# Performance work log

Hardware: AMD Instinct MI355X
Metric: run time of the kernel (lower is better)

Reference implementation:

```python
import jax, jax.numpy as jnp
import numpy as np

B, H, W, C = 16, 256, 256, 3
K_MAX = 64


def setup_inputs() -> dict:
    key = jax.random.key(0)
    k1, k2, k3 = jax.random.split(key, 3)
    images = jax.random.uniform(k1, (B, H, W, C), dtype=jnp.float32)
    palettes = jax.random.uniform(k2, (B, K_MAX, C), dtype=jnp.float32)
    # ragged palette sizes in [1, K_MAX]; entries >= size are padding
    palette_sizes = jax.random.randint(k3, (B,), 1, K_MAX + 1, dtype=jnp.int32)
    temperature = jnp.float32(1.0)
    return {"images": images, "palettes": palettes,
            "palette_sizes": palette_sizes, "temperature": temperature}


def reference(images, palettes, palette_sizes, temperature):
    # valid-entry mask emulating the ragged [B, (K), C] palette
    mask = jnp.arange(K_MAX)[None, :] < palette_sizes[:, None]          # [B, K]
    # per-pixel squared distance to each palette color: [B, H, W, K]
    diff = images[:, :, :, None, :] - palettes[:, None, None, :, :]
    distances = jnp.sum(diff * diff, axis=-1)
    logits = -distances / temperature
    # padded palette slots get -inf logits -> zero softmax weight,
    # exactly matching the ragged softmax over K_i entries
    logits = jnp.where(mask[:, None, None, :], logits, -jnp.inf)
    weights = jax.nn.softmax(logits, axis=-1)                            # [B, H, W, K]
    # softmax-weighted color blend (padded slots contribute 0)
    return jnp.einsum('bhwk,bkc->bhwc', weights, palettes)
```

## Files before the change

### kernel.cpp

```cpp
#include <hip/hip_runtime.h>


#define BATCH 16
#define HW 65536
#define KMAX 64
#define BLOCKS_PER_IMG 256

__global__ __launch_bounds__(64) void coef_kernel(
    const float* __restrict__ palettes,
    const float* __restrict__ temperature,
    float*       __restrict__ cf)
{
    const int b = blockIdx.x;
    const int k = threadIdx.x;
    const float invT  = 1.0f / temperature[0];
    const float scale = invT * 1.4426950408889634f;

    const float pr = palettes[(b * KMAX + k) * 3 + 0];
    const float pg = palettes[(b * KMAX + k) * 3 + 1];
    const float pb = palettes[(b * KMAX + k) * 3 + 2];

    float* o = cf + ((long)(b * KMAX + k) << 3);
    o[0] = 2.0f * pr * scale;
    o[1] = 2.0f * pg * scale;
    o[2] = 2.0f * pb * scale;
    o[3] = (-(pr * pr + pg * pg + pb * pb) - 3.0f) * scale;
    o[4] = pr;
    o[5] = pg;
    o[6] = pb;
    o[7] = 0.0f;
}

__global__ __launch_bounds__(256) void palette_blend_kernel(
    const float* __restrict__ images,
    const int*   __restrict__ palette_sizes,
    const float* __restrict__ cf,
    float*       __restrict__ out)
{
    const int b   = blockIdx.x >> 8;
    const int pix = ((blockIdx.x & (BLOCKS_PER_IMG - 1)) << 8) + threadIdx.x;
    const int K   = palette_sizes[b];

    const long base = (long)b * (HW * 3) + (long)pix * 3;
    const float x0 = images[base + 0];
    const float x1 = images[base + 1];
    const float x2 = images[base + 2];

    const float4* __restrict__ c4 = (const float4*)(cf + ((long)b * KMAX << 3));

    float s = 0.0f, o0 = 0.0f, o1 = 0.0f, o2 = 0.0f;
    #pragma unroll 4
    for (int k = 0; k < K; ++k) {
        const float4 A = c4[2 * k];
        const float4 P = c4[2 * k + 1];
        const float l2 = fmaf(A.x, x0, fmaf(A.y, x1, fmaf(A.z, x2, A.w)));
        const float w  = exp2f(l2);
        s  += w;
        o0 = fmaf(w, P.x, o0);
        o1 = fmaf(w, P.y, o1);
        o2 = fmaf(w, P.z, o2);
    }

    const float inv = 1.0f / s;
    out[base + 0] = o0 * inv;
    out[base + 1] = o1 * inv;
    out[base + 2] = o2 * inv;
}

extern "C" void kernel_launch(void* const* d_in, const int* in_sizes, int n_in,
                              void* d_out, int out_size, void* d_ws, size_t ws_size,
                              hipStream_t stream) {
    const float* images        = (const float*)d_in[0];
    const float* palettes      = (const float*)d_in[1];
    const int*   palette_sizes = (const int*)d_in[2];
    const float* temperature   = (const float*)d_in[3];
    float*       out           = (float*)d_out;
    float*       cf            = (float*)d_ws;

    coef_kernel<<<dim3(BATCH), dim3(KMAX), 0, stream>>>(palettes, temperature, cf);
    palette_blend_kernel<<<dim3(BATCH * BLOCKS_PER_IMG), dim3(256), 0, stream>>>(
        images, palette_sizes, cf, out);
}
```

Measured before the change: 84.14 us.

## Move palette coefficients to constant memory and drop duplicate palette colors

```diff
diff --git a/kernel.cpp b/kernel.cpp
--- a/kernel.cpp
+++ b/kernel.cpp
@@ -5,6 +5,9 @@
 #define HW 65536
 #define KMAX 64
 #define BLOCKS_PER_IMG 256
+#define CF_ELEMS (BATCH * KMAX * 4)
+
+__constant__ float cf_const[CF_ELEMS];
 
 __global__ __launch_bounds__(64) void coef_kernel(
     const float* __restrict__ palettes,
@@ -13,28 +16,23 @@
 {
     const int b = blockIdx.x;
     const int k = threadIdx.x;
-    const float invT  = 1.0f / temperature[0];
-    const float scale = invT * 1.4426950408889634f;
+    const float scale = 1.4426950408889634f / temperature[0];
 
     const float pr = palettes[(b * KMAX + k) * 3 + 0];
     const float pg = palettes[(b * KMAX + k) * 3 + 1];
     const float pb = palettes[(b * KMAX + k) * 3 + 2];
 
-    float* o = cf + ((long)(b * KMAX + k) << 3);
+    float* o = cf + ((b * KMAX + k) << 2);
     o[0] = 2.0f * pr * scale;
     o[1] = 2.0f * pg * scale;
     o[2] = 2.0f * pb * scale;
     o[3] = (-(pr * pr + pg * pg + pb * pb) - 3.0f) * scale;
-    o[4] = pr;
-    o[5] = pg;
-    o[6] = pb;
-    o[7] = 0.0f;
 }
 
 __global__ __launch_bounds__(256) void palette_blend_kernel(
     const float* __restrict__ images,
     const int*   __restrict__ palette_sizes,
-    const float* __restrict__ cf,
+    const float* __restrict__ temperature,
     float*       __restrict__ out)
 {
     const int b   = blockIdx.x >> 8;
@@ -46,22 +44,25 @@
     const float x1 = images[base + 1];
     const float x2 = images[base + 2];
 
-    const float4* __restrict__ c4 = (const float4*)(cf + ((long)b * KMAX << 3));
+    const int cbase = (b * KMAX) << 2;
 
     float s = 0.0f, o0 = 0.0f, o1 = 0.0f, o2 = 0.0f;
     #pragma unroll 4
     for (int k = 0; k < K; ++k) {
-        const float4 A = c4[2 * k];
-        const float4 P = c4[2 * k + 1];
-        const float l2 = fmaf(A.x, x0, fmaf(A.y, x1, fmaf(A.z, x2, A.w)));
-        const float w  = exp2f(l2);
+        const float a0 = cf_const[cbase + (k << 2) + 0];
+        const float a1 = cf_const[cbase + (k << 2) + 1];
+        const float a2 = cf_const[cbase + (k << 2) + 2];
+        const float c  = cf_const[cbase + (k << 2) + 3];
+        const float l  = fmaf(a0, x0, fmaf(a1, x1, fmaf(a2, x2, c)));
+        const float w  = exp2f(l);
         s  += w;
-        o0 = fmaf(w, P.x, o0);
-        o1 = fmaf(w, P.y, o1);
-        o2 = fmaf(w, P.z, o2);
+        o0 = fmaf(w, a0, o0);
+        o1 = fmaf(w, a1, o1);
+        o2 = fmaf(w, a2, o2);
     }
 
-    const float inv = 1.0f / s;
+    const float scale = 1.4426950408889634f / temperature[0];
+    const float inv   = 1.0f / (s * 2.0f * scale);
     out[base + 0] = o0 * inv;
     out[base + 1] = o1 * inv;
     out[base + 2] = o2 * inv;
@@ -77,7 +78,12 @@
     float*       out           = (float*)d_out;
     float*       cf            = (float*)d_ws;
 
+    void* sym = nullptr;
+    (void)hipGetSymbolAddress(&sym, HIP_SYMBOL(cf_const));
+
     coef_kernel<<<dim3(BATCH), dim3(KMAX), 0, stream>>>(palettes, temperature, cf);
+    (void)hipMemcpyAsync(sym, cf, CF_ELEMS * sizeof(float),
+                         hipMemcpyDeviceToDevice, stream);
     palette_blend_kernel<<<dim3(BATCH * BLOCKS_PER_IMG), dim3(256), 0, stream>>>(
-        images, palette_sizes, cf, out);
+        images, palette_sizes, temperature, out);
 }
```

Measured after the change: 85.70 us. About the same (+1.9%).
